# Optimization experiments

Hardware: AMD Instinct MI355X
Metric: run time of the kernel (lower is better)

Reference implementation:

```python
import jax, jax.numpy as jnp
import numpy as np

N, E = 20000, 320000
IN_DIM = 18            # 2 (pos) + k_feat=16
P = 32                 # in_proj_out
H1, D1 = 8, 32         # gat1 heads, head_dim (out_dim = P*heads = 256)
OUT = P * H1           # 256
BD, H2, D2 = 256, 8, 32  # bottleneck dim / heads / head_dim
NID = 1000             # num_real_ids
NEG_SLOPE = 0.2


def _ln(x, g, b, eps=1e-5):
    mu = x.mean(-1, keepdims=True)
    v = ((x - mu) ** 2).mean(-1, keepdims=True)
    return (x - mu) * jax.lax.rsqrt(v + eps) * g + b


def _segment_softmax(score, dst, n):
    # score: [E, H], softmax over edges sharing the same dst node
    m = jax.ops.segment_max(score, dst, num_segments=n)
    e = jnp.exp(score - m[dst])
    s = jax.ops.segment_sum(e, dst, num_segments=n)
    return e / (s[dst] + 1e-16)


def _gatv2(x, src, dst, ea, Wl, Wr, We, att, bias, n, h, d):
    # GATv2 (PyG semantics): e_ij = att . leaky_relu(Wl x_j + Wr x_i + We e_ij)
    xl = (x @ Wl).reshape(n, h, d)           # source transform
    xr = (x @ Wr).reshape(n, h, d)           # target transform
    xe = (ea @ We).reshape(-1, h, d)         # edge embedding [E,h,d]
    f = jax.nn.leaky_relu(xl[src] + xr[dst] + xe, NEG_SLOPE)  # [E,h,d]
    score = jnp.einsum('ehd,hd->eh', f, att)                   # [E,h]
    alpha = _segment_softmax(score, dst, n)                    # [E,h]
    out = jax.ops.segment_sum(alpha[:, :, None] * xl[src], dst, num_segments=n)
    return out.reshape(n, h * d) + bias


def setup_inputs() -> dict:
    key = jax.random.key(0)
    ks = jax.random.split(key, 20)
    s = 0.05
    rn = lambda k, shape: (jax.random.normal(k, shape, jnp.float32) * s)
    return {
        'x_gnn': jax.random.normal(ks[0], (N, IN_DIM), jnp.float32),
        'edge_index': jax.random.randint(ks[1], (2, E), 0, N),
        'edge_attr': jax.random.uniform(ks[2], (E, 1), dtype=jnp.float32),
        'W_in': rn(ks[3], (IN_DIM, P)), 'b_in': jnp.zeros((P,), jnp.float32),
        'Wl1': rn(ks[4], (P, OUT)), 'Wr1': rn(ks[5], (P, OUT)),
        'We1': rn(ks[6], (1, OUT)), 'att1': rn(ks[7], (H1, D1)),
        'bg1': jnp.zeros((OUT,), jnp.float32),
        'ln1_g': jnp.ones((OUT,), jnp.float32), 'ln1_b': jnp.zeros((OUT,), jnp.float32),
        'W_down': rn(ks[8], (OUT, BD)),
        'lnd_g': jnp.ones((BD,), jnp.float32), 'lnd_b': jnp.zeros((BD,), jnp.float32),
        'Wl2': rn(ks[9], (BD, BD)), 'Wr2': rn(ks[10], (BD, BD)),
        'We2': rn(ks[11], (1, BD)), 'att2': rn(ks[12], (H2, D2)),
        'bg2': jnp.zeros((BD,), jnp.float32),
        'ln2_g': jnp.ones((BD,), jnp.float32), 'ln2_b': jnp.zeros((BD,), jnp.float32),
        'W_up': rn(ks[13], (BD, OUT)),
        'lnu_g': jnp.ones((OUT,), jnp.float32), 'lnu_b': jnp.zeros((OUT,), jnp.float32),
        'W_cls': rn(ks[14], (OUT, NID)), 'b_cls': jnp.zeros((NID,), jnp.float32),
    }


def reference(x_gnn, edge_index, edge_attr, W_in, b_in,
              Wl1, Wr1, We1, att1, bg1, ln1_g, ln1_b,
              W_down, lnd_g, lnd_b,
              Wl2, Wr2, We2, att2, bg2, ln2_g, ln2_b,
              W_up, lnu_g, lnu_b, W_cls, b_cls):
    src, dst = edge_index[0], edge_index[1]
    h0 = x_gnn @ W_in + b_in
    # GATv2Block 1: conv + LN (no residual, 32 -> 256)
    g1 = _gatv2(h0, src, dst, edge_attr, Wl1, Wr1, We1, att1, bg1, N, H1, D1)
    h1 = _ln(g1, ln1_g, ln1_b)
    # bottleneck branch
    z = _ln(h1 @ W_down, lnd_g, lnd_b)
    # GATv2Block 2: conv + residual + LN (256 -> 256)
    g2 = _gatv2(z, src, dst, edge_attr, Wl2, Wr2, We2, att2, bg2, N, H2, D2)
    z2 = _ln(g2 + z, ln2_g, ln2_b)
    h2 = z2 @ W_up                       # up projection (dropout is identity in eval)
    h = _ln(h1 + h2, lnu_g, lnu_b)
    logits = h @ W_cls + b_cls
    return (logits, h)
```

## Files before the change

### kernel.cpp

```cpp
#include <hip/hip_runtime.h>
#include <math.h>

#define N_NODES 20000
#define N_EDGES 320000

typedef __attribute__((ext_vector_type(8))) __bf16 bf16x8;
typedef __attribute__((ext_vector_type(8))) unsigned short ushort8;
typedef __attribute__((ext_vector_type(4))) float floatx4;

__device__ __forceinline__ unsigned short f2b(float f) {
    unsigned int u = __float_as_uint(f);
    unsigned int r = (u + 0x7fffu + ((u >> 16) & 1u)) >> 16;
    return (unsigned short)r;
}
__device__ __forceinline__ float b2f(unsigned short u) {
    return __uint_as_float(((unsigned int)u) << 16);
}

__global__ void k_prep(const float* __restrict__ x, const float* __restrict__ Wi,
                       const float* __restrict__ bi, unsigned short* __restrict__ h0,
                       const int* __restrict__ dst, int* __restrict__ cnt,
                       const float* __restrict__ Wl1, const float* __restrict__ Wr1,
                       const float* __restrict__ Wdn, const float* __restrict__ Wl2,
                       const float* __restrict__ Wr2, const float* __restrict__ Wup,
                       const float* __restrict__ Wcl,
                       unsigned short* __restrict__ o1, unsigned short* __restrict__ o2,
                       unsigned short* __restrict__ o3, unsigned short* __restrict__ o4,
                       unsigned short* __restrict__ o5, unsigned short* __restrict__ o6,
                       unsigned short* __restrict__ o7) {
    int t = blockIdx.x * blockDim.x + threadIdx.x;
    if (t < 640000) {
        int n = t >> 5, p = t & 31;
        float acc = bi[p];
        const float* xr = x + n * 18;
#pragma unroll
        for (int k = 0; k < 18; k++) acc = fmaf(xr[k], Wi[k * 32 + p], acc);
        h0[t] = f2b(acc);
        return;
    }
    if (t < 960000) {
        atomicAdd(cnt + dst[t - 640000], 1);
        return;
    }
    int u = t - 960000;
    const float* W; unsigned short* O; int Nd, K, idx;
    if (u < 8192)        { W = Wl1; O = o1; Nd = 256;  K = 32;  idx = u; }
    else if (u < 16384)  { W = Wr1; O = o2; Nd = 256;  K = 32;  idx = u - 8192; }
    else if (u < 81920)  { W = Wdn; O = o3; Nd = 256;  K = 256; idx = u - 16384; }
    else if (u < 147456) { W = Wl2; O = o4; Nd = 256;  K = 256; idx = u - 81920; }
    else if (u < 212992) { W = Wr2; O = o5; Nd = 256;  K = 256; idx = u - 147456; }
    else if (u < 278528) { W = Wup; O = o6; Nd = 256;  K = 256; idx = u - 212992; }
    else if (u < 540672) { W = Wcl; O = o7; Nd = 1000; K = 256; idx = u - 278528; }
    else return;
    int n = idx / K, k = idx % K;
    float v = (n < Nd) ? W[(size_t)k * Nd + n] : 0.f;
    O[idx] = f2b(v);
}

__global__ __launch_bounds__(256) void k_gemm_bf16(
    const unsigned short* __restrict__ A, const unsigned short* __restrict__ Bt,
    float* __restrict__ Cf, unsigned short* __restrict__ Cb,
    const float* __restrict__ bias, int M, int N, int K) {
    __shared__ unsigned short As[8 * 64 * 8];
    __shared__ unsigned short Bs[8 * 64 * 8];
    int tid = threadIdx.x;
    int wave = tid >> 6, lane = tid & 63;
    int wr = wave >> 1, wc = wave & 1;
    int row0 = blockIdx.x * 128, col0 = blockIdx.y * 128;
    floatx4 zero4 = {0.f, 0.f, 0.f, 0.f};
    floatx4 acc[4][4];
#pragma unroll
    for (int i = 0; i < 4; i++)
#pragma unroll
        for (int j = 0; j < 4; j++) acc[i][j] = zero4;
    for (int kb = 0; kb < K; kb += 32) {
#pragma unroll
        for (int q = 0; q < 2; q++) {
            int c = tid * 2 + q;
            int row = c >> 2, koff = (c & 3) * 8;
            int lp = (row & 15) + 16 * (koff >> 3);
            int mt = row >> 4;
            ushort8 va = {0, 0, 0, 0, 0, 0, 0, 0};
            if (row0 + row < M)
                va = *(const ushort8*)(A + (size_t)(row0 + row) * K + kb + koff);
            *(ushort8*)(As + (mt * 64 + lp) * 8) = va;
            ushort8 vb = {0, 0, 0, 0, 0, 0, 0, 0};
            if (col0 + row < N)
                vb = *(const ushort8*)(Bt + (size_t)(col0 + row) * K + kb + koff);
            *(ushort8*)(Bs + (mt * 64 + lp) * 8) = vb;
        }
        __syncthreads();
        bf16x8 af[4], bfr[4];
#pragma unroll
        for (int i = 0; i < 4; i++)
            af[i] = *(const bf16x8*)(As + ((wr * 4 + i) * 64 + lane) * 8);
#pragma unroll
        for (int j = 0; j < 4; j++)
            bfr[j] = *(const bf16x8*)(Bs + ((wc * 4 + j) * 64 + lane) * 8);
#pragma unroll
        for (int i = 0; i < 4; i++)
#pragma unroll
            for (int j = 0; j < 4; j++)
                acc[i][j] = __builtin_amdgcn_mfma_f32_16x16x32_bf16(
                    af[i], bfr[j], acc[i][j], 0, 0, 0);
        __syncthreads();
    }
    int quad = lane >> 4, nl = lane & 15;
#pragma unroll
    for (int i = 0; i < 4; i++) {
#pragma unroll
        for (int j = 0; j < 4; j++) {
            int col = col0 + wc * 64 + j * 16 + nl;
            if (col >= N) continue;
            float bv = bias ? bias[col] : 0.f;
#pragma unroll
            for (int r = 0; r < 4; r++) {
                int rr = row0 + wr * 64 + i * 16 + quad * 4 + r;
                if (rr >= M) continue;
                float v = acc[i][j][r] + bv;
                if (Cf) Cf[(size_t)rr * N + col] = v;
                else Cb[(size_t)rr * N + col] = f2b(v);
            }
        }
    }
}

__global__ __launch_bounds__(512) void k_gemm_stride(
    const unsigned short* __restrict__ A,
    const unsigned short* __restrict__ Bt,
    int Ncols, int ldC,
    const float* __restrict__ bias,
    const float* __restrict__ res,
    const float* __restrict__ g, const float* __restrict__ b,
    float* __restrict__ outf, unsigned short* __restrict__ outb) {
    __shared__ unsigned short As[2][16 * 256];
    __shared__ float red[8][16][2];
    int tid = threadIdx.x, lane = tid & 63, wave = tid >> 6;
    int nl = lane & 15, quad = lane >> 4;
    int cbase = blockIdx.y * 256 + wave * 32;
    int sr = tid >> 5, sc = tid & 31;
    int swz = (sc ^ (sr & 7)) << 3;
    int R = gridDim.x;

    bf16x8 breg[2][8];
    const unsigned short* bptr = Bt + (size_t)(cbase + nl) * 256 + quad * 8;
#pragma unroll
    for (int j = 0; j < 2; j++)
#pragma unroll
        for (int kb = 0; kb < 8; kb++)
            breg[j][kb] = *(const bf16x8*)(bptr + j * 16 * 256 + kb * 32);

    int s = blockIdx.x;
    {
        ushort8 v = *(const ushort8*)(A + ((size_t)s * 16 + sr) * 256 + sc * 8);
        *(ushort8*)(&As[0][sr * 256 + swz]) = v;
    }
    __syncthreads();
    int p = 0;
    while (s < 1250) {
        int snext = s + R;
        bool more = (snext < 1250);
        ushort8 av;
        if (more)
            av = *(const ushort8*)(A + ((size_t)snext * 16 + sr) * 256 + sc * 8);

        floatx4 acc0 = {0.f, 0.f, 0.f, 0.f};
        floatx4 acc1 = {0.f, 0.f, 0.f, 0.f};
#pragma unroll
        for (int kb = 0; kb < 8; kb++) {
            int kq = kb * 4 + quad;
            bf16x8 a = *(const bf16x8*)(&As[p][nl * 256 + (((kq ^ (nl & 7))) << 3)]);
            acc0 = __builtin_amdgcn_mfma_f32_16x16x32_bf16(a, breg[0][kb], acc0, 0, 0, 0);
            acc1 = __builtin_amdgcn_mfma_f32_16x16x32_bf16(a, breg[1][kb], acc1, 0, 0, 0);
        }
        int row0 = s * 16;

        if (g == nullptr) {
#pragma unroll
            for (int j = 0; j < 2; j++) {
                int col = cbase + j * 16 + nl;
                if (col < Ncols) {
                    float bv = bias ? bias[col] : 0.f;
                    floatx4 aj = j ? acc1 : acc0;
#pragma unroll
                    for (int r = 0; r < 4; r++) {
                        int rr = row0 + quad * 4 + r;
                        float v = aj[r] + bv;
                        if (outf) outf[(size_t)rr * ldC + col] = v;
                        if (outb) outb[(size_t)rr * ldC + col] = f2b(v);
                    }
                }
            }
        } else {
            if (res) {
#pragma unroll
                for (int r = 0; r < 4; r++) {
                    int rr = row0 + quad * 4 + r;
                    acc0[r] += res[(size_t)rr * 256 + cbase + nl];
                    acc1[r] += res[(size_t)rr * 256 + cbase + 16 + nl];
                }
            }
#pragma unroll
            for (int r = 0; r < 4; r++) {
                float su = acc0[r] + acc1[r];
                float q = fmaf(acc0[r], acc0[r], acc1[r] * acc1[r]);
                su += __shfl_xor(su, 1, 64); q += __shfl_xor(q, 1, 64);
                su += __shfl_xor(su, 2, 64); q += __shfl_xor(q, 2, 64);
                su += __shfl_xor(su, 4, 64); q += __shfl_xor(q, 4, 64);
                su += __shfl_xor(su, 8, 64); q += __shfl_xor(q, 8, 64);
                if (nl == 0) {
                    red[wave][quad * 4 + r][0] = su;
                    red[wave][quad * 4 + r][1] = q;
                }
            }
            __syncthreads();
            float mean_[4], rstd_[4];
#pragma unroll
            for (int r = 0; r < 4; r++) {
                int row = quad * 4 + r;
                float su = 0.f, q = 0.f;
#pragma unroll
                for (int w = 0; w < 8; w++) { su += red[w][row][0]; q += red[w][row][1]; }
                float mean = su * (1.0f / 256.0f);
                float var = q * (1.0f / 256.0f) - mean * mean;
                mean_[r] = mean;
                rstd_[r] = 1.0f / sqrtf(var + 1e-5f);
            }
#pragma unroll
            for (int j = 0; j < 2; j++) {
                int col = cbase + j * 16 + nl;
                float gv = g[col], bvv = b[col];
                floatx4 aj = j ? acc1 : acc0;
#pragma unroll
                for (int r = 0; r < 4; r++) {
                    int rr = row0 + quad * 4 + r;
                    float o = (aj[r] - mean_[r]) * rstd_[r] * gv + bvv;
                    if (outf) outf[(size_t)rr * 256 + col] = o;
                    if (outb) outb[(size_t)rr * 256 + col] = f2b(o);
                }
            }
        }

        if (more) *(ushort8*)(&As[p ^ 1][sr * 256 + swz]) = av;
        __syncthreads();
        p ^= 1;
        s = snext;
    }
}

__global__ __launch_bounds__(1024) void k_scan(const int* __restrict__ cnt,
                                               int* __restrict__ rowptr,
                                               int* __restrict__ wp, int n) {
    __shared__ int tsum[1024];
    int t = threadIdx.x;
    const int chunk = 20;
    int i0 = t * chunk;
    int local[chunk];
    int s = 0;
#pragma unroll
    for (int j = 0; j < chunk; j++) {
        int i = i0 + j;
        int v = (i < n) ? cnt[i] : 0;
        local[j] = s;
        s += v;
    }
    tsum[t] = s;
    __syncthreads();
    for (int off = 1; off < 1024; off <<= 1) {
        int other = (t >= off) ? tsum[t - off] : 0;
        __syncthreads();
        tsum[t] += other;
        __syncthreads();
    }
    int base = (t > 0) ? tsum[t - 1] : 0;
#pragma unroll
    for (int j = 0; j < chunk; j++) {
        int i = i0 + j;
        if (i < n) {
            int ex = base + local[j];
            rowptr[i] = ex;
            wp[i] = ex;
        }
    }
    if (t == 1023) rowptr[n] = tsum[1023];
}

__global__ void k_fill(const int* __restrict__ src, const int* __restrict__ dst,
                       const float* __restrict__ ea, int* __restrict__ wp,
                       int* __restrict__ srcs, float* __restrict__ eas) {
    int e = blockIdx.x * blockDim.x + threadIdx.x;
    if (e >= N_EDGES) return;
    int p = atomicAdd(wp + dst[e], 1);
    srcs[p] = src[e];
    eas[p] = ea[e];
}

__global__ __launch_bounds__(256) void k_gat_ln(
    const int* __restrict__ rowptr, const int* __restrict__ srcs,
    const float* __restrict__ eas, const unsigned short* __restrict__ xlr,
    const float* __restrict__ We, const float* __restrict__ att,
    const float* __restrict__ vbias, const float* __restrict__ res,
    const float* __restrict__ g, const float* __restrict__ b,
    float* __restrict__ outf, unsigned short* __restrict__ outb) {
    int node = blockIdx.x * 4 + (threadIdx.x >> 6);
    if (node >= N_NODES) return;
    int lane = threadIdx.x & 63;
    int beg = rowptr[node], end = rowptr[node + 1];
    float4 wv = ((const float4*)We)[lane];
    float4 av = ((const float4*)att)[lane];
    ushort4 xru = ((const ushort4*)(xlr + (size_t)node * 512 + 256))[lane];
    float4 rv = make_float4(b2f(xru.x), b2f(xru.y), b2f(xru.z), b2f(xru.w));
    float m = -3.0e38f, l = 0.f;
    float4 acc = make_float4(0.f, 0.f, 0.f, 0.f);
    if (beg < end) {
        int last = end - 1;
        int i1 = (beg + 1 < end) ? beg + 1 : last;
        int i2 = (beg + 2 < end) ? beg + 2 : last;
        int i3 = (beg + 3 < end) ? beg + 3 : last;
        int i4 = (beg + 4 < end) ? beg + 4 : last;
        int i5 = (beg + 5 < end) ? beg + 5 : last;
        int i6 = (beg + 6 < end) ? beg + 6 : last;
        int i7 = (beg + 7 < end) ? beg + 7 : last;
        int i8 = (beg + 8 < end) ? beg + 8 : last;
        int i9 = (beg + 9 < end) ? beg + 9 : last;
        int s0a = srcs[beg], s0b = srcs[i1];
        int s1a = srcs[i2],  s1b = srcs[i3];
        int s2a = srcs[i4],  s2b = srcs[i5];
        int s3a = srcs[i6],  s3b = srcs[i7];
        int s4a = srcs[i8],  s4b = srcs[i9];
        float a0a = eas[beg], a0b = eas[i1];
        float a1a = eas[i2],  a1b = eas[i3];
        float a2a = eas[i4],  a2b = eas[i5];
        float a3a = eas[i6],  a3b = eas[i7];
        float a4a = eas[i8],  a4b = eas[i9];
        ushort4 x0a = ((const ushort4*)(xlr + (size_t)s0a * 512))[lane];
        ushort4 x0b = ((const ushort4*)(xlr + (size_t)s0b * 512))[lane];
        ushort4 x1a = ((const ushort4*)(xlr + (size_t)s1a * 512))[lane];
        ushort4 x1b = ((const ushort4*)(xlr + (size_t)s1b * 512))[lane];
        ushort4 x2a = ((const ushort4*)(xlr + (size_t)s2a * 512))[lane];
        ushort4 x2b = ((const ushort4*)(xlr + (size_t)s2b * 512))[lane];
        ushort4 x3a = ((const ushort4*)(xlr + (size_t)s3a * 512))[lane];
        ushort4 x3b = ((const ushort4*)(xlr + (size_t)s3b * 512))[lane];
        for (int i = beg; i < end; i += 2) {
            int j10 = (i + 10 < end) ? i + 10 : last;
            int j11 = (i + 11 < end) ? i + 11 : last;
            int s5a = srcs[j10], s5b = srcs[j11];
            float a5a = eas[j10], a5b = eas[j11];
            ushort4 x4a = ((const ushort4*)(xlr + (size_t)s4a * 512))[lane];
            ushort4 x4b = ((const ushort4*)(xlr + (size_t)s4b * 512))[lane];
            float4 lva = make_float4(b2f(x0a.x), b2f(x0a.y), b2f(x0a.z), b2f(x0a.w));
            float4 lvb = make_float4(b2f(x0b.x), b2f(x0b.y), b2f(x0b.z), b2f(x0b.w));
            float f, pa = 0.f, pb = 0.f;
            f = lva.x + rv.x + a0a * wv.x; f = fmaxf(f, 0.2f * f); pa = fmaf(f, av.x, pa);
            f = lva.y + rv.y + a0a * wv.y; f = fmaxf(f, 0.2f * f); pa = fmaf(f, av.y, pa);
            f = lva.z + rv.z + a0a * wv.z; f = fmaxf(f, 0.2f * f); pa = fmaf(f, av.z, pa);
            f = lva.w + rv.w + a0a * wv.w; f = fmaxf(f, 0.2f * f); pa = fmaf(f, av.w, pa);
            f = lvb.x + rv.x + a0b * wv.x; f = fmaxf(f, 0.2f * f); pb = fmaf(f, av.x, pb);
            f = lvb.y + rv.y + a0b * wv.y; f = fmaxf(f, 0.2f * f); pb = fmaf(f, av.y, pb);
            f = lvb.z + rv.z + a0b * wv.z; f = fmaxf(f, 0.2f * f); pb = fmaf(f, av.z, pb);
            f = lvb.w + rv.w + a0b * wv.w; f = fmaxf(f, 0.2f * f); pb = fmaf(f, av.w, pb);
            pa += __shfl_xor(pa, 1, 64);
            pa += __shfl_xor(pa, 2, 64);
            pa += __shfl_xor(pa, 4, 64);
            pb += __shfl_xor(pb, 1, 64);
            pb += __shfl_xor(pb, 2, 64);
            pb += __shfl_xor(pb, 4, 64);
            if (i + 1 >= end) pb = -3.0e38f;
            float mnew = fmaxf(fmaxf(m, pa), pb);
            float scale = __expf(m - mnew);
            float wa = __expf(pa - mnew);
            float wb = __expf(pb - mnew);
            acc.x = fmaf(acc.x, scale, fmaf(wa, lva.x, wb * lvb.x));
            acc.y = fmaf(acc.y, scale, fmaf(wa, lva.y, wb * lvb.y));
            acc.z = fmaf(acc.z, scale, fmaf(wa, lva.z, wb * lvb.z));
            acc.w = fmaf(acc.w, scale, fmaf(wa, lva.w, wb * lvb.w));
            l = fmaf(l, scale, wa + wb);
            m = mnew;
            x0a = x1a; x0b = x1b; x1a = x2a; x1b = x2b;
            x2a = x3a; x2b = x3b; x3a = x4a; x3b = x4b;
            a0a = a1a; a0b = a1b; a1a = a2a; a1b = a2b;
            a2a = a3a; a2b = a3b; a3a = a4a; a3b = a4b;
            a4a = a5a; a4b = a5b; s4a = s5a; s4b = s5b;
        }
    }
    float inv = 1.0f / (l + 1e-16f);
    float4 vb4 = ((const float4*)vbias)[lane];
    float4 o = make_float4(fmaf(acc.x, inv, vb4.x), fmaf(acc.y, inv, vb4.y),
                           fmaf(acc.z, inv, vb4.z), fmaf(acc.w, inv, vb4.w));
    if (res) {
        float4 r4 = ((const float4*)(res + (size_t)node * 256))[lane];
        o.x += r4.x; o.y += r4.y; o.z += r4.z; o.w += r4.w;
    }
    float sum = o.x + o.y + o.z + o.w;
#pragma unroll
    for (int off = 32; off > 0; off >>= 1) sum += __shfl_xor(sum, off, 64);
    float mean = sum * (1.0f / 256.0f);
    float dx = o.x - mean, dy = o.y - mean, dz = o.z - mean, dw = o.w - mean;
    float sq = dx * dx + dy * dy + dz * dz + dw * dw;
#pragma unroll
    for (int off = 32; off > 0; off >>= 1) sq += __shfl_xor(sq, off, 64);
    float rstd = 1.0f / sqrtf(sq * (1.0f / 256.0f) + 1e-5f);
    float4 gg = ((const float4*)g)[lane];
    float4 bb = ((const float4*)b)[lane];
    float4 o4 = make_float4(dx * rstd * gg.x + bb.x, dy * rstd * gg.y + bb.y,
                            dz * rstd * gg.z + bb.z, dw * rstd * gg.w + bb.w);
    if (outf) ((float4*)(outf + (size_t)node * 256))[lane] = o4;
    if (outb) {
        ushort4 u;
        u.x = f2b(o4.x); u.y = f2b(o4.y); u.z = f2b(o4.z); u.w = f2b(o4.w);
        ((ushort4*)(outb + (size_t)node * 256))[lane] = u;
    }
}

extern "C" void kernel_launch(void* const* d_in, const int* in_sizes, int n_in,
                              void* d_out, int out_size, void* d_ws, size_t ws_size,
                              hipStream_t stream) {
    const float* x_gnn = (const float*)d_in[0];
    const int* ei = (const int*)d_in[1];
    const int* src = ei;
    const int* dst = ei + N_EDGES;
    const float* ea   = (const float*)d_in[2];
    const float* W_in = (const float*)d_in[3];
    const float* b_in = (const float*)d_in[4];
    const float* Wl1  = (const float*)d_in[5];
    const float* Wr1  = (const float*)d_in[6];
    const float* We1  = (const float*)d_in[7];
    const float* att1 = (const float*)d_in[8];
    const float* bg1  = (const float*)d_in[9];
    const float* ln1_g = (const float*)d_in[10];
    const float* ln1_b = (const float*)d_in[11];
    const float* W_down = (const float*)d_in[12];
    const float* lnd_g = (const float*)d_in[13];
    const float* lnd_b = (const float*)d_in[14];
    const float* Wl2  = (const float*)d_in[15];
    const float* Wr2  = (const float*)d_in[16];
    const float* We2  = (const float*)d_in[17];
    const float* att2 = (const float*)d_in[18];
    const float* bg2  = (const float*)d_in[19];
    const float* ln2_g = (const float*)d_in[20];
    const float* ln2_b = (const float*)d_in[21];
    const float* W_up = (const float*)d_in[22];
    const float* lnu_g = (const float*)d_in[23];
    const float* lnu_b = (const float*)d_in[24];
    const float* W_cls = (const float*)d_in[25];
    const float* b_cls = (const float*)d_in[26];

    float* ws = (float*)d_ws;
    float* B_agg = ws;
    float* B_h1  = B_agg + 5120000;
    float* B_z   = B_h1 + 5120000;
    unsigned short* B_xlr = (unsigned short*)(B_z + 5120000);
    unsigned short* B_actb = B_xlr + 10240000;
    unsigned short* B_h0b = B_actb + 5120000;
    unsigned short* Wt_l1 = B_h0b + 640000;
    unsigned short* Wt_r1 = Wt_l1 + 8192;
    unsigned short* Wt_down = Wt_r1 + 8192;
    unsigned short* Wt_l2 = Wt_down + 65536;
    unsigned short* Wt_r2 = Wt_l2 + 65536;
    unsigned short* Wt_up = Wt_r2 + 65536;
    unsigned short* Wt_cls = Wt_up + 65536;
    int* C_cnt = (int*)(Wt_cls + 262144);
    int* C_row = C_cnt + 20000;
    int* C_wp  = C_row + 20001;
    int* C_src = C_wp + 20000;
    float* C_ea = (float*)(C_src + 320000);

    float* out_logits = (float*)d_out;
    float* out_h = out_logits + (size_t)N_NODES * 1000;

    int gatblk = (N_NODES + 3) / 4;
    dim3 gl((N_NODES + 127) / 128, 4);

    hipMemsetAsync(C_cnt, 0, (size_t)20000 * 4, stream);
    k_prep<<<5862, 256, 0, stream>>>(x_gnn, W_in, b_in, B_h0b, dst, C_cnt,
                                     Wl1, Wr1, W_down, Wl2, Wr2, W_up, W_cls,
                                     Wt_l1, Wt_r1, Wt_down, Wt_l2, Wt_r2, Wt_up, Wt_cls);
    k_scan<<<1, 1024, 0, stream>>>(C_cnt, C_row, C_wp, N_NODES);
    k_fill<<<(N_EDGES + 255) / 256, 256, 0, stream>>>(src, dst, ea, C_wp, C_src, C_ea);

    k_gemm_bf16<<<gl, 256, 0, stream>>>(B_h0b, Wt_l1, nullptr, B_xlr, nullptr, N_NODES, 512, 32);
    k_gat_ln<<<gatblk, 256, 0, stream>>>(C_row, C_src, C_ea, B_xlr, We1, att1,
                                         bg1, nullptr, ln1_g, ln1_b, B_h1, B_actb);
    k_gemm_stride<<<dim3(512, 1), 512, 0, stream>>>(
        B_actb, Wt_down, 256, 256, nullptr, nullptr, lnd_g, lnd_b, B_z, B_actb);
    k_gemm_stride<<<dim3(256, 2), 512, 0, stream>>>(
        B_actb, Wt_l2, 512, 512, nullptr, nullptr, nullptr, nullptr, nullptr, B_xlr);
    k_gat_ln<<<gatblk, 256, 0, stream>>>(C_row, C_src, C_ea, B_xlr, We2, att2,
                                         bg2, B_z, ln2_g, ln2_b, nullptr, B_actb);
    k_gemm_stride<<<dim3(512, 1), 512, 0, stream>>>(
        B_actb, Wt_up, 256, 256, nullptr, B_h1, lnu_g, lnu_b, out_h, B_actb);
    k_gemm_stride<<<dim3(128, 4), 512, 0, stream>>>(
        B_actb, Wt_cls, 1000, 1000, b_cls, nullptr, nullptr, nullptr,
        out_logits, nullptr);
}
```

Baseline: 402.1 us.

## Fuse down-projection LN with layer-2 GAT projections; store residuals as bf16

Adds a fused kernel that computes the down projection, applies its LayerNorm, stages the normalized tile in shared memory, and runs the Wl2/Wr2 projection directly from it. This removes one launch and the round trip of the bottleneck activations through global memory. The h1 and z residual buffers are now kept in bf16 instead of fp32, which halves residual read/write traffic. The cost is lower precision on the residual paths and recomputing the down GEMM in both y-blocks of the fused grid.

Measured after the change: 395.3 us. No clear change (-1.7%).

```diff
diff --git a/kernel.cpp b/kernel.cpp
--- a/kernel.cpp
+++ b/kernel.cpp
@@ -130,7 +130,7 @@
     const unsigned short* __restrict__ Bt,
     int Ncols, int ldC,
     const float* __restrict__ bias,
-    const float* __restrict__ res,
+    const unsigned short* __restrict__ res,
     const float* __restrict__ g, const float* __restrict__ b,
     float* __restrict__ outf, unsigned short* __restrict__ outb) {
     __shared__ unsigned short As[2][16 * 256];
@@ -196,8 +196,8 @@
 #pragma unroll
                 for (int r = 0; r < 4; r++) {
                     int rr = row0 + quad * 4 + r;
-                    acc0[r] += res[(size_t)rr * 256 + cbase + nl];
-                    acc1[r] += res[(size_t)rr * 256 + cbase + 16 + nl];
+                    acc0[r] += b2f(res[(size_t)rr * 256 + cbase + nl]);
+                    acc1[r] += b2f(res[(size_t)rr * 256 + cbase + 16 + nl]);
                 }
             }
 #pragma unroll
@@ -248,6 +248,127 @@
     }
 }
 
+__global__ __launch_bounds__(512) void k_fuse(
+    const unsigned short* __restrict__ A,
+    const unsigned short* __restrict__ Bdn,
+    const unsigned short* __restrict__ B2base,
+    const float* __restrict__ g, const float* __restrict__ b,
+    unsigned short* __restrict__ zb,
+    unsigned short* __restrict__ xlr) {
+    __shared__ unsigned short As[2][16 * 256];
+    __shared__ unsigned short Zs[16 * 256];
+    __shared__ float red[8][16][2];
+    int tid = threadIdx.x, lane = tid & 63, wave = tid >> 6;
+    int nl = lane & 15, quad = lane >> 4;
+    int sr = tid >> 5, sc = tid & 31;
+    int swz = (sc ^ (sr & 7)) << 3;
+    int ybase = blockIdx.y * 256;
+    const unsigned short* B2 = B2base + (size_t)blockIdx.y * 65536;
+
+    bf16x8 b1[2][8];
+    const unsigned short* p1 = Bdn + (size_t)(wave * 32 + nl) * 256 + quad * 8;
+#pragma unroll
+    for (int j = 0; j < 2; j++)
+#pragma unroll
+        for (int kb = 0; kb < 8; kb++)
+            b1[j][kb] = *(const bf16x8*)(p1 + j * 16 * 256 + kb * 32);
+    bf16x8 b2[2][8];
+    const unsigned short* p2 = B2 + (size_t)(wave * 32 + nl) * 256 + quad * 8;
+#pragma unroll
+    for (int j = 0; j < 2; j++)
+#pragma unroll
+        for (int kb = 0; kb < 8; kb++)
+            b2[j][kb] = *(const bf16x8*)(p2 + j * 16 * 256 + kb * 32);
+
+    int s = blockIdx.x;
+    {
+        ushort8 v = *(const ushort8*)(A + ((size_t)s * 16 + sr) * 256 + sc * 8);
+        *(ushort8*)(&As[0][sr * 256 + swz]) = v;
+    }
+    __syncthreads();
+    int p = 0;
+    while (s < 1250) {
+        int snext = s + 125;
+        bool more = (snext < 1250);
+        ushort8 av;
+        if (more)
+            av = *(const ushort8*)(A + ((size_t)snext * 16 + sr) * 256 + sc * 8);
+
+        floatx4 acc0 = {0.f, 0.f, 0.f, 0.f};
+        floatx4 acc1 = {0.f, 0.f, 0.f, 0.f};
+#pragma unroll
+        for (int kb = 0; kb < 8; kb++) {
+            int kq = kb * 4 + quad;
+            bf16x8 a = *(const bf16x8*)(&As[p][nl * 256 + ((kq ^ (nl & 7)) << 3)]);
+            acc0 = __builtin_amdgcn_mfma_f32_16x16x32_bf16(a, b1[0][kb], acc0, 0, 0, 0);
+            acc1 = __builtin_amdgcn_mfma_f32_16x16x32_bf16(a, b1[1][kb], acc1, 0, 0, 0);
+        }
+        int row0 = s * 16;
+#pragma unroll
+        for (int r = 0; r < 4; r++) {
+            float su = acc0[r] + acc1[r];
+            float q = fmaf(acc0[r], acc0[r], acc1[r] * acc1[r]);
+            su += __shfl_xor(su, 1, 64); q += __shfl_xor(q, 1, 64);
+            su += __shfl_xor(su, 2, 64); q += __shfl_xor(q, 2, 64);
+            su += __shfl_xor(su, 4, 64); q += __shfl_xor(q, 4, 64);
+            su += __shfl_xor(su, 8, 64); q += __shfl_xor(q, 8, 64);
+            if (nl == 0) {
+                red[wave][quad * 4 + r][0] = su;
+                red[wave][quad * 4 + r][1] = q;
+            }
+        }
+        __syncthreads();
+        float mean_[4], rstd_[4];
+#pragma unroll
+        for (int r = 0; r < 4; r++) {
+            int row = quad * 4 + r;
+            float su = 0.f, q = 0.f;
+#pragma unroll
+            for (int w = 0; w < 8; w++) { su += red[w][row][0]; q += red[w][row][1]; }
+            float mean = su * (1.0f / 256.0f);
+            float var = q * (1.0f / 256.0f) - mean * mean;
+            mean_[r] = mean;
+            rstd_[r] = 1.0f / sqrtf(var + 1e-5f);
+        }
+#pragma unroll
+        for (int j = 0; j < 2; j++) {
+            int col = wave * 32 + j * 16 + nl;
+            float gv = g[col], bvv = b[col];
+            floatx4 aj = j ? acc1 : acc0;
+#pragma unroll
+            for (int r = 0; r < 4; r++) {
+                int rl = quad * 4 + r;
+                float zv = (aj[r] - mean_[r]) * rstd_[r] * gv + bvv;
+                unsigned short us = f2b(zv);
+                Zs[rl * 256 + (((col >> 3) ^ (rl & 7)) << 3) + (col & 7)] = us;
+                if (blockIdx.y == 0) zb[(size_t)(row0 + rl) * 256 + col] = us;
+            }
+        }
+        __syncthreads();
+        floatx4 c0 = {0.f, 0.f, 0.f, 0.f};
+        floatx4 c1 = {0.f, 0.f, 0.f, 0.f};
+#pragma unroll
+        for (int kb = 0; kb < 8; kb++) {
+            int kq = kb * 4 + quad;
+            bf16x8 a = *(const bf16x8*)(&Zs[nl * 256 + ((kq ^ (nl & 7)) << 3)]);
+            c0 = __builtin_amdgcn_mfma_f32_16x16x32_bf16(a, b2[0][kb], c0, 0, 0, 0);
+            c1 = __builtin_amdgcn_mfma_f32_16x16x32_bf16(a, b2[1][kb], c1, 0, 0, 0);
+        }
+#pragma unroll
+        for (int j = 0; j < 2; j++) {
+            int col = ybase + wave * 32 + j * 16 + nl;
+            floatx4 cj = j ? c1 : c0;
+#pragma unroll
+            for (int r = 0; r < 4; r++)
+                xlr[(size_t)(row0 + quad * 4 + r) * 512 + col] = f2b(cj[r]);
+        }
+        if (more) *(ushort8*)(&As[p ^ 1][sr * 256 + swz]) = av;
+        __syncthreads();
+        p ^= 1;
+        s = snext;
+    }
+}
+
 __global__ __launch_bounds__(1024) void k_scan(const int* __restrict__ cnt,
                                                int* __restrict__ rowptr,
                                                int* __restrict__ wp, int n) {
@@ -299,7 +420,7 @@
     const int* __restrict__ rowptr, const int* __restrict__ srcs,
     const float* __restrict__ eas, const unsigned short* __restrict__ xlr,
     const float* __restrict__ We, const float* __restrict__ att,
-    const float* __restrict__ vbias, const float* __restrict__ res,
+    const float* __restrict__ vbias, const unsigned short* __restrict__ res,
     const float* __restrict__ g, const float* __restrict__ b,
     float* __restrict__ outf, unsigned short* __restrict__ outb) {
     int node = blockIdx.x * 4 + (threadIdx.x >> 6);
@@ -388,8 +509,8 @@
     float4 o = make_float4(fmaf(acc.x, inv, vb4.x), fmaf(acc.y, inv, vb4.y),
                            fmaf(acc.z, inv, vb4.z), fmaf(acc.w, inv, vb4.w));
     if (res) {
-        float4 r4 = ((const float4*)(res + (size_t)node * 256))[lane];
-        o.x += r4.x; o.y += r4.y; o.z += r4.z; o.w += r4.w;
+        ushort4 r4 = ((const ushort4*)(res + (size_t)node * 256))[lane];
+        o.x += b2f(r4.x); o.y += b2f(r4.y); o.z += b2f(r4.z); o.w += b2f(r4.w);
     }
     float sum = o.x + o.y + o.z + o.w;
 #pragma unroll
@@ -445,11 +566,9 @@
     const float* W_cls = (const float*)d_in[25];
     const float* b_cls = (const float*)d_in[26];
 
-    float* ws = (float*)d_ws;
-    float* B_agg = ws;
-    float* B_h1  = B_agg + 5120000;
-    float* B_z   = B_h1 + 5120000;
-    unsigned short* B_xlr = (unsigned short*)(B_z + 5120000);
+    unsigned short* B_h1b = (unsigned short*)d_ws;
+    unsigned short* B_zb  = B_h1b + 5120000;
+    unsigned short* B_xlr = B_zb + 5120000;
     unsigned short* B_actb = B_xlr + 10240000;
     unsigned short* B_h0b = B_actb + 5120000;
     unsigned short* Wt_l1 = B_h0b + 640000;
@@ -480,15 +599,13 @@
 
     k_gemm_bf16<<<gl, 256, 0, stream>>>(B_h0b, Wt_l1, nullptr, B_xlr, nullptr, N_NODES, 512, 32);
     k_gat_ln<<<gatblk, 256, 0, stream>>>(C_row, C_src, C_ea, B_xlr, We1, att1,
-                                         bg1, nullptr, ln1_g, ln1_b, B_h1, B_actb);
+                                         bg1, nullptr, ln1_g, ln1_b, nullptr, B_h1b);
+    k_fuse<<<dim3(125, 2), 512, 0, stream>>>(B_h1b, Wt_down, Wt_l2,
+                                             lnd_g, lnd_b, B_zb, B_xlr);
+    k_gat_ln<<<gatblk, 256, 0, stream>>>(C_row, C_src, C_ea, B_xlr, We2, att2,
+                                         bg2, B_zb, ln2_g, ln2_b, nullptr, B_actb);
     k_gemm_stride<<<dim3(512, 1), 512, 0, stream>>>(
-        B_actb, Wt_down, 256, 256, nullptr, nullptr, lnd_g, lnd_b, B_z, B_actb);
-    k_gemm_stride<<<dim3(256, 2), 512, 0, stream>>>(
-        B_actb, Wt_l2, 512, 512, nullptr, nullptr, nullptr, nullptr, nullptr, B_xlr);
-    k_gat_ln<<<gatblk, 256, 0, stream>>>(C_row, C_src, C_ea, B_xlr, We2, att2,
-                                         bg2, B_z, ln2_g, ln2_b, nullptr, B_actb);
-    k_gemm_stride<<<dim3(512, 1), 512, 0, stream>>>(
-        B_actb, Wt_up, 256, 256, nullptr, B_h1, lnu_g, lnu_b, out_h, B_actb);
+        B_actb, Wt_up, 256, 256, nullptr, B_h1b, lnu_g, lnu_b, out_h, B_actb);
     k_gemm_stride<<<dim3(128, 4), 512, 0, stream>>>(
         B_actb, Wt_cls, 1000, 1000, b_cls, nullptr, nullptr, nullptr,
         out_logits, nullptr);
```
